# Performance work log

Measured on AMD Instinct MI355X. Metric: run time of the kernel, lower is better.

The kernel has to match this reference:

```python
import jax, jax.numpy as jnp
import numpy as np

B, N = 4, 1024
DIM, DEPTH, HEADS, DHEAD, MLP = 512, 6, 8, 64, 2048
INNER = HEADS * DHEAD
SCALE = DHEAD ** -0.5
EPS = 1e-5


def setup_inputs() -> dict:
    key = jax.random.key(0)
    ks = jax.random.split(key, 16)
    w = lambda k, shape: (jax.random.normal(k, shape, jnp.float32) * 0.02)
    D = DEPTH
    return {
        "g": jax.random.normal(ks[0], (B, N, DIM), jnp.float32),
        "x": jax.random.normal(ks[1], (B, N, DIM), jnp.float32),
        # PreNorm + SelfAttention
        "ln1_s": jnp.ones((D, DIM)), "ln1_b": jnp.zeros((D, DIM)),
        "Wqkv": w(ks[2], (D, DIM, 3 * INNER)),
        "Wo_sa": w(ks[3], (D, INNER, DIM)), "bo_sa": jnp.zeros((D, DIM)),
        # RelationalCrossAttention
        "lng_s": jnp.ones((D, DIM)), "lng_b": jnp.zeros((D, DIM)),
        "lnx_s": jnp.ones((D, DIM)), "lnx_b": jnp.zeros((D, DIM)),
        "Wq": w(ks[4], (D, DIM, INNER)),
        "Wk": w(ks[5], (D, DIM, INNER)),
        "Wv": w(ks[6], (D, DIM, INNER)), "bv": jnp.zeros((D, INNER)),
        "Wo_ca": w(ks[7], (D, INNER, DIM)), "bo_ca": jnp.zeros((D, DIM)),
        # PreNorm + FeedForward (same module applied twice per layer)
        "lnf_s": jnp.ones((D, DIM)), "lnf_b": jnp.zeros((D, DIM)),
        "W1": w(ks[8], (D, DIM, MLP)), "b1": jnp.zeros((D, MLP)),
        "W2": w(ks[9], (D, MLP, DIM)), "b2": jnp.zeros((D, DIM)),
    }


def _ln(t, s, b):
    m = t.mean(-1, keepdims=True)
    v = ((t - m) ** 2).mean(-1, keepdims=True)
    return (t - m) / jnp.sqrt(v + EPS) * s + b


def _split_heads(t):  # [b, n, h*d] -> [b, h, n, d]
    b, n, _ = t.shape
    return t.reshape(b, n, HEADS, DHEAD).transpose(0, 2, 1, 3)


def _merge_heads(t):  # [b, h, n, d] -> [b, n, h*d]
    b, h, n, d = t.shape
    return t.transpose(0, 2, 1, 3).reshape(b, n, h * d)


def _attend(q, k, v):
    dots = jnp.einsum('bhnd,bhmd->bhnm', q, k) * SCALE
    attn = jax.nn.softmax(jnp.nan_to_num(dots, nan=-jnp.inf), axis=-1)
    attn = jnp.nan_to_num(attn)  # nan_to_num(0.0) post-softmax as in source
    return jnp.einsum('bhnm,bhmd->bhnd', attn, jnp.nan_to_num(v))


def reference(g, x, ln1_s, ln1_b, Wqkv, Wo_sa, bo_sa, lng_s, lng_b, lnx_s, lnx_b,
              Wq, Wk, Wv, bv, Wo_ca, bo_ca, lnf_s, lnf_b, W1, b1, W2, b2):
    for i in range(DEPTH):
        def ff(t):
            h = jax.nn.gelu(_ln(t, lnf_s[i], lnf_b[i]) @ W1[i] + b1[i], approximate=False)
            return h @ W2[i] + b2[i]
        # relational cross attention: q,k from g, v from x
        gn = _ln(g, lng_s[i], lng_b[i])
        xn = _ln(x, lnx_s[i], lnx_b[i])
        q = _split_heads(gn @ Wq[i])
        k = _split_heads(gn @ Wk[i])
        v = _split_heads(xn @ Wv[i] + bv[i])
        x = _merge_heads(_attend(q, k, v)) @ Wo_ca[i] + bo_ca[i] + x
        x = ff(x) + x
        # pre-norm self attention (skip connection enabled)
        sn = _ln(x, ln1_s[i], ln1_b[i])
        qkv = sn @ Wqkv[i]
        qs, ks_, vs = jnp.split(qkv, 3, axis=-1)
        sa = _merge_heads(_attend(_split_heads(qs), _split_heads(ks_), _split_heads(vs)))
        x = sa @ Wo_sa[i] + bo_sa[i] + x
        x = ff(x) + x
    return x
```

## Files before the change

kernel.cpp:

```cpp
#include <hip/hip_runtime.h>
#include <hip/hip_bf16.h>
#include <cstdint>
#include <cstddef>

#define DEV __device__ __forceinline__

using f32x4 = __attribute__((ext_vector_type(4))) float;
using bfx8  = __attribute__((ext_vector_type(8))) __bf16;
using s16x8 = __attribute__((ext_vector_type(8))) short;

DEV uint16_t f2bf(float f) {
    union { float f; uint32_t u; } x; x.f = f;
    uint32_t r = x.u + 0x7fffu + ((x.u >> 16) & 1u);
    return (uint16_t)(r >> 16);
}

DEV float gelu_exact(float v) {
    return 0.5f * v * (1.0f + erff(v * 0.70710678118654752f));
}

DEV f32x4 mfma16(s16x8 a, s16x8 b, f32x4 c) {
    return __builtin_amdgcn_mfma_f32_16x16x32_bf16(
        __builtin_bit_cast(bfx8, a), __builtin_bit_cast(bfx8, b), c, 0, 0, 0);
}

DEV void async_lds16(const void* g, void* l) {
    __builtin_amdgcn_global_load_lds(
        (const __attribute__((address_space(1))) uint32_t*)g,
        (__attribute__((address_space(3))) uint32_t*)l, 16, 0, 0);
}

template<int N> DEV void wait_vmcnt() {
    if constexpr (N == 0)      asm volatile("s_waitcnt vmcnt(0)" ::: "memory");
    else if constexpr (N == 4) asm volatile("s_waitcnt vmcnt(4)" ::: "memory");
    else static_assert(N == 0 || N == 4, "add vmcnt literal");
}
#define SBAR      asm volatile("s_barrier" ::: "memory")
#define LGKM0     asm volatile("s_waitcnt lgkmcnt(0)" ::: "memory")
#define SCHED0    __builtin_amdgcn_sched_barrier(0)

DEV void ln_row(const float* __restrict__ in, const float* __restrict__ sc,
                const float* __restrict__ bi, uint16_t* __restrict__ out, size_t row)
{
    const int lane = threadIdx.x & 63;
    const float* p = in + row * 512 + lane * 8;
    float4 a = *(const float4*)p;
    float4 b4 = *(const float4*)(p + 4);
    float v[8] = {a.x, a.y, a.z, a.w, b4.x, b4.y, b4.z, b4.w};
    float s = 0.f, sq = 0.f;
#pragma unroll
    for (int j = 0; j < 8; ++j) { s += v[j]; sq += v[j] * v[j]; }
#pragma unroll
    for (int o = 1; o < 64; o <<= 1) { s += __shfl_xor(s, o); sq += __shfl_xor(sq, o); }
    const float mean = s * (1.0f / 512.0f);
    const float var  = sq * (1.0f / 512.0f) - mean * mean;
    const float rstd = rsqrtf(var + 1e-5f);
    const int c = lane * 8;
    uint16_t o8[8];
#pragma unroll
    for (int j = 0; j < 8; ++j)
        o8[j] = f2bf((v[j] - mean) * rstd * sc[c + j] + bi[c + j]);
    uint4 pk;
    pk.x = (uint32_t)o8[0] | ((uint32_t)o8[1] << 16);
    pk.y = (uint32_t)o8[2] | ((uint32_t)o8[3] << 16);
    pk.z = (uint32_t)o8[4] | ((uint32_t)o8[5] << 16);
    pk.w = (uint32_t)o8[6] | ((uint32_t)o8[7] << 16);
    *reinterpret_cast<uint4*>(out + row * 512 + c) = pk;
}

__global__ __launch_bounds__(256)
void ln_bf16(const float* __restrict__ in, const float* __restrict__ sc,
             const float* __restrict__ bi, uint16_t* __restrict__ out)
{
    ln_row(in, sc, bi, out, (size_t)blockIdx.x * 4 + (threadIdx.x >> 6));
}

__global__ __launch_bounds__(256)
void ln2_bf16(const float* __restrict__ in0, const float* __restrict__ sc0,
              const float* __restrict__ bi0, uint16_t* __restrict__ out0,
              const float* __restrict__ in1, const float* __restrict__ sc1,
              const float* __restrict__ bi1, uint16_t* __restrict__ out1)
{
    const int sel = blockIdx.x >> 10;
    const size_t row = (size_t)(blockIdx.x & 1023) * 4 + (threadIdx.x >> 6);
    if (sel == 0) ln_row(in0, sc0, bi0, out0, row);
    else          ln_row(in1, sc1, bi1, out1, row);
}

__global__ __launch_bounds__(256)
void wtrans(const float* __restrict__ W, uint16_t* __restrict__ WT, int K, int N,
            size_t lstride, int row0)
{
    __shared__ float tile[32][33];
    const int l = blockIdx.z;
    const int k0 = blockIdx.x * 32, n0 = blockIdx.y * 32;
    const float* Wl = W + (size_t)l * K * N;
    uint16_t* WTl = WT + (size_t)l * lstride;
    const int tx = threadIdx.x, ty = threadIdx.y;
#pragma unroll
    for (int j = 0; j < 4; ++j)
        tile[ty + j * 8][tx] = Wl[(size_t)(k0 + ty + j * 8) * N + n0 + tx];
    __syncthreads();
#pragma unroll
    for (int j = 0; j < 4; ++j)
        WTl[(size_t)(row0 + n0 + ty + j * 8) * K + k0 + tx] = f2bf(tile[tx][ty + j * 8]);
}

__global__ __launch_bounds__(256)
void vtrans(const uint16_t* __restrict__ src, uint16_t* __restrict__ vt, int C, int coff)
{
    __shared__ uint16_t tile[64][72];
    const int n0 = blockIdx.x * 64;
    const int bh = blockIdx.y, b = bh >> 3, h = bh & 7;
    const int tx = threadIdx.x, ty = threadIdx.y;
#pragma unroll
    for (int j = 0; j < 16; ++j) {
        const int n = ty + j * 4;
        tile[n][tx] = src[((size_t)b * 1024 + n0 + n) * C + coff + h * 64 + tx];
    }
    __syncthreads();
    uint16_t* o = vt + (size_t)bh * 65536;
#pragma unroll
    for (int j = 0; j < 16; ++j) {
        const int d = ty + j * 4;
        o[(size_t)d * 1024 + n0 + tx] = tile[tx][d];
    }
}

template<int BM, int BN, int NWR, int NWC, int MINW,
         int HAS_BIAS, int HAS_RESID, int DO_GELU, int OUT_BF16, int PARTIAL>
__global__ __launch_bounds__(NWR * NWC * 64, MINW)
void gemm5(const uint16_t* __restrict__ A, const uint16_t* __restrict__ BT,
           const float* __restrict__ bias, const float* __restrict__ resid,
           void* __restrict__ outp, int M, int N, int K, int kh)
{
    constexpr int NT = NWR * NWC * 64;
    constexpr int WM = BM / NWR, WN = BN / NWC;
    constexpr int FM = WM / 16, FN = WN / 16;
    constexpr int ASLOTS = 8 * BM, BSLOTS = 8 * BN, TOT = ASLOTS + BSLOTS;
    constexpr int S = TOT / NT;
    static_assert(S == 4, "vmcnt literal assumes S==4");
    __shared__ uint16_t As[2][ASLOTS * 8];
    __shared__ uint16_t Bs[2][BSLOTS * 8];
    const int tid = threadIdx.x, lane = tid & 63;
    const int w = tid >> 6, wr = w / NWC, wc = w % NWC;
    const int kg = lane >> 4, lr = lane & 15;
    const int nwg = gridDim.x;
    const int id0 = blockIdx.x;
    const int id = (id0 & 7) * (nwg >> 3) + (id0 >> 3);
    const int nbn = N / BN;
    const size_t m0 = (size_t)(id / nbn) * BM;
    const size_t n0 = (size_t)(id % nbn) * BN;
    const int kbase = PARTIAL ? blockIdx.y * kh : 0;

    auto stage = [&](int b, int k0) {
#pragma unroll
        for (int j = 0; j < S; ++j) {
            const int s = j * NT + tid;
            if (s < ASLOTS) {
                const int sub = s / BM, row = s % BM;
                async_lds16(A + (m0 + row) * K + k0 + sub * 8, &As[b][s * 8]);
            } else {
                const int s2 = s - ASLOTS;
                const int sub = s2 / BN, row = s2 % BN;
                async_lds16(BT + (n0 + row) * K + k0 + sub * 8, &Bs[b][s2 * 8]);
            }
        }
    };

    f32x4 acc[FM][FN] = {};
    const int nt = kh / 64;
    stage(0, kbase);
    stage(1, kbase + 64);
    int cur = 0;
    for (int t = 0; t < nt; ++t) {
        if (t < nt - 1) wait_vmcnt<S>(); else wait_vmcnt<0>();
        SBAR;
        s16x8 af[2][FM], bf[2][FN];
#pragma unroll
        for (int ks = 0; ks < 2; ++ks) {
#pragma unroll
            for (int i = 0; i < FM; ++i)
                af[ks][i] = *(const s16x8*)&As[cur][((ks * 4 + kg) * BM + wr * WM + i * 16 + lr) * 8];
#pragma unroll
            for (int j = 0; j < FN; ++j)
                bf[ks][j] = *(const s16x8*)&Bs[cur][((ks * 4 + kg) * BN + wc * WN + j * 16 + lr) * 8];
        }
        __builtin_amdgcn_s_setprio(1);
#pragma unroll
        for (int ks = 0; ks < 2; ++ks)
#pragma unroll
            for (int i = 0; i < FM; ++i)
#pragma unroll
                for (int j = 0; j < FN; ++j)
                    acc[i][j] = mfma16(af[ks][i], bf[ks][j], acc[i][j]);
        __builtin_amdgcn_s_setprio(0);
        LGKM0; SCHED0;
        SBAR;
        if (t + 2 < nt) stage(cur, kbase + (t + 2) * 64);
        cur ^= 1;
    }
    float* pout = PARTIAL ? (float*)outp + (size_t)blockIdx.y * M * (size_t)N : nullptr;
#pragma unroll
    for (int i = 0; i < FM; ++i) {
        const size_t rbase = m0 + wr * WM + i * 16 + kg * 4;
#pragma unroll
        for (int j = 0; j < FN; ++j) {
            const size_t col = n0 + wc * WN + j * 16 + lr;
            const float bval = HAS_BIAS ? bias[col] : 0.0f;
#pragma unroll
            for (int r = 0; r < 4; ++r) {
                const size_t row = rbase + r;
                float v = acc[i][j][r] + bval;
                if (PARTIAL) { pout[row * (size_t)N + col] = v; continue; }
                if (DO_GELU)  v = gelu_exact(v);
                if (HAS_RESID) v += resid[row * (size_t)N + col];
                if (OUT_BF16) ((uint16_t*)outp)[row * (size_t)N + col] = f2bf(v);
                else          ((float*)outp)[row * (size_t)N + col] = v;
            }
        }
    }
}

__global__ __launch_bounds__(256)
void reduce2(const float* __restrict__ p, const float* __restrict__ bias,
             float* __restrict__ x)
{
    const size_t i = ((size_t)blockIdx.x * 256 + threadIdx.x) * 8;
    const int col = (int)(i & 511);
    const float* q = p + 4096ull * 512;
    float4 a0 = *(const float4*)(p + i),     a1 = *(const float4*)(p + i + 4);
    float4 b0 = *(const float4*)(q + i),     b1 = *(const float4*)(q + i + 4);
    float4 s0 = *(const float4*)(bias + col), s1 = *(const float4*)(bias + col + 4);
    float4 r0 = *(const float4*)(x + i),     r1 = *(const float4*)(x + i + 4);
    float4 o0, o1;
    o0.x = a0.x + b0.x + s0.x + r0.x;  o0.y = a0.y + b0.y + s0.y + r0.y;
    o0.z = a0.z + b0.z + s0.z + r0.z;  o0.w = a0.w + b0.w + s0.w + r0.w;
    o1.x = a1.x + b1.x + s1.x + r1.x;  o1.y = a1.y + b1.y + s1.y + r1.y;
    o1.z = a1.z + b1.z + s1.z + r1.z;  o1.w = a1.w + b1.w + s1.w + r1.w;
    *(float4*)(x + i) = o0;
    *(float4*)(x + i + 4) = o1;
}

__global__ __launch_bounds__(256)
void attn_flash(const uint16_t* __restrict__ Qb, const uint16_t* __restrict__ Kb,
                const uint16_t* __restrict__ Vt, uint16_t* __restrict__ Ob,
                int qstride, int kstride, int qoff, int koff)
{
    __shared__ uint16_t Ks[2][4096];
    __shared__ uint16_t Vs[2][4096];
    __shared__ uint16_t Pb[4][1024];
    const int tid = threadIdx.x, lane = tid & 63, w = tid >> 6;
    const int kg = lane >> 4, lr = lane & 15;
    const int bh = blockIdx.y, b = bh >> 3, h = bh & 7;
    const int q0 = blockIdx.x * 64;
    const float CEXP = 0.125f * 1.44269504f;

    s16x8 aq0, aq1;
    {
        const size_t qrow = (size_t)b * 1024 + q0 + w * 16 + lr;
        const uint16_t* qp = Qb + qrow * qstride + qoff + h * 64 + kg * 8;
        aq0 = *(const s16x8*)qp;
        aq1 = *(const s16x8*)(qp + 32);
    }
    const uint16_t* kbase = Kb + (size_t)b * 1024 * kstride + koff + h * 64;
    const uint16_t* vbase = Vt + (size_t)bh * 65536;

    float l_r[4] = {0.f, 0.f, 0.f, 0.f};
    f32x4 acc[4] = {};

    auto stage = [&](int buf, int kv0) {
#pragma unroll
        for (int j = 0; j < 2; ++j) {
            const int s = j * 256 + tid;
            const int sub = s >> 6, row = s & 63;
            async_lds16(kbase + (size_t)(kv0 + row) * kstride + sub * 8, &Ks[buf][s * 8]);
            async_lds16(vbase + (size_t)row * 1024 + kv0 + sub * 8,      &Vs[buf][s * 8]);
        }
    };

    stage(0, 0);
    __syncthreads();
    int cur = 0;
    for (int t = 0; t < 16; ++t) {
        if (t < 15) stage(cur ^ 1, (t + 1) * 64);
        f32x4 s4[4];
        __builtin_amdgcn_s_setprio(1);
#pragma unroll
        for (int ni = 0; ni < 4; ++ni) {
            s16x8 bk0 = *(const s16x8*)&Ks[cur][(kg * 64 + ni * 16 + lr) * 8];
            s16x8 bk1 = *(const s16x8*)&Ks[cur][((4 + kg) * 64 + ni * 16 + lr) * 8];
            f32x4 z = {};
            z = mfma16(aq0, bk0, z);
            z = mfma16(aq1, bk1, z);
            s4[ni] = z;
        }
        __builtin_amdgcn_s_setprio(0);
#pragma unroll
        for (int ni = 0; ni < 4; ++ni) {
            const int slotb = (ni * 2 + (lr >> 3)) * 16 + kg * 4;
#pragma unroll
            for (int r = 0; r < 4; ++r) {
                const float pe = __builtin_amdgcn_exp2f(s4[ni][r] * CEXP);
                l_r[r] += pe;
                Pb[w][(slotb + r) * 8 + (lr & 7)] = f2bf(pe);
            }
        }
        s16x8 ap0 = *(const s16x8*)&Pb[w][(kg * 16 + lr) * 8];
        s16x8 ap1 = *(const s16x8*)&Pb[w][((4 + kg) * 16 + lr) * 8];
        __builtin_amdgcn_s_setprio(1);
#pragma unroll
        for (int ni = 0; ni < 4; ++ni) {
            s16x8 bv0 = *(const s16x8*)&Vs[cur][(kg * 64 + ni * 16 + lr) * 8];
            s16x8 bv1 = *(const s16x8*)&Vs[cur][((4 + kg) * 64 + ni * 16 + lr) * 8];
            acc[ni] = mfma16(ap0, bv0, acc[ni]);
            acc[ni] = mfma16(ap1, bv1, acc[ni]);
        }
        __builtin_amdgcn_s_setprio(0);
        __syncthreads();
        cur ^= 1;
    }
    float linv[4];
#pragma unroll
    for (int r = 0; r < 4; ++r) {
        float l = l_r[r];
        l += __shfl_xor(l, 1); l += __shfl_xor(l, 2);
        l += __shfl_xor(l, 4); l += __shfl_xor(l, 8);
        linv[r] = 1.0f / l;
    }
#pragma unroll
    for (int ni = 0; ni < 4; ++ni)
#pragma unroll
        for (int r = 0; r < 4; ++r) {
            const float v = acc[ni][r] * linv[r];
            const size_t row = (size_t)b * 1024 + q0 + w * 16 + kg * 4 + r;
            Ob[row * 512 + h * 64 + ni * 16 + lr] = f2bf(v);
        }
}

extern "C" void kernel_launch(void* const* d_in, const int* in_sizes, int n_in,
                              void* d_out, int out_size, void* d_ws, size_t ws_size,
                              hipStream_t stream)
{
    (void)in_sizes; (void)n_in; (void)out_size; (void)ws_size;
    const float* g     = (const float*)d_in[0];
    const float* x0    = (const float*)d_in[1];
    const float* ln1_s = (const float*)d_in[2];
    const float* ln1_b = (const float*)d_in[3];
    const float* Wqkv  = (const float*)d_in[4];
    const float* Wo_sa = (const float*)d_in[5];
    const float* bo_sa = (const float*)d_in[6];
    const float* lng_s = (const float*)d_in[7];
    const float* lng_b = (const float*)d_in[8];
    const float* lnx_s = (const float*)d_in[9];
    const float* lnx_b = (const float*)d_in[10];
    const float* Wq    = (const float*)d_in[11];
    const float* Wk    = (const float*)d_in[12];
    const float* Wv    = (const float*)d_in[13];
    const float* bv    = (const float*)d_in[14];
    const float* Wo_ca = (const float*)d_in[15];
    const float* bo_ca = (const float*)d_in[16];
    const float* lnf_s = (const float*)d_in[17];
    const float* lnf_b = (const float*)d_in[18];
    const float* W1    = (const float*)d_in[19];
    const float* b1    = (const float*)d_in[20];
    const float* W2    = (const float*)d_in[21];
    const float* b2    = (const float*)d_in[22];

    float* x = (float*)d_out;

    char* p = (char*)d_ws;
    auto carve = [&](size_t n) { char* r = p; p += (n + 255) & ~(size_t)255; return r; };
    uint16_t* WqkT  = (uint16_t*)carve(6ull * 1024 * 512 * 2);
    uint16_t* WvT   = (uint16_t*)carve(6ull * 512 * 512 * 2);
    uint16_t* WocaT = (uint16_t*)carve(6ull * 512 * 512 * 2);
    uint16_t* WqkvT = (uint16_t*)carve(6ull * 1536 * 512 * 2);
    uint16_t* WosaT = (uint16_t*)carve(6ull * 512 * 512 * 2);
    uint16_t* W1T   = (uint16_t*)carve(6ull * 2048 * 512 * 2);
    uint16_t* W2T   = (uint16_t*)carve(6ull * 512 * 2048 * 2);
    uint16_t* gn    = (uint16_t*)carve(4096ull * 512 * 2);
    uint16_t* xn    = (uint16_t*)carve(4096ull * 512 * 2);
    uint16_t* qkvu  = (uint16_t*)carve(4096ull * 1536 * 2);
    uint16_t* vt    = (uint16_t*)carve(32ull * 64 * 1024 * 2);
    uint16_t* ab    = (uint16_t*)carve(4096ull * 512 * 2);
    uint16_t* hb    = (uint16_t*)carve(4096ull * 2048 * 2);
    float*    pk2   = (float*)carve(2ull * 4096 * 512 * 4);
    uint16_t* qk = qkvu;
    uint16_t* vb = qkvu + 4096ull * 1024;

    dim3 tb(32, 8);
    wtrans<<<dim3(16, 16, 6), tb, 0, stream>>>(Wq,    WqkT,  512, 512,  1024ull * 512, 0);
    wtrans<<<dim3(16, 16, 6), tb, 0, stream>>>(Wk,    WqkT,  512, 512,  1024ull * 512, 512);
    wtrans<<<dim3(16, 16, 6), tb, 0, stream>>>(Wv,    WvT,   512, 512,  512ull * 512, 0);
    wtrans<<<dim3(16, 16, 6), tb, 0, stream>>>(Wo_ca, WocaT, 512, 512,  512ull * 512, 0);
    wtrans<<<dim3(16, 48, 6), tb, 0, stream>>>(Wqkv,  WqkvT, 512, 1536, 1536ull * 512, 0);
    wtrans<<<dim3(16, 16, 6), tb, 0, stream>>>(Wo_sa, WosaT, 512, 512,  512ull * 512, 0);
    wtrans<<<dim3(16, 64, 6), tb, 0, stream>>>(W1,    W1T,   512, 2048, 2048ull * 512, 0);
    wtrans<<<dim3(64, 16, 6), tb, 0, stream>>>(W2,    W2T,   2048, 512, 2048ull * 512, 0);

    hipMemcpyAsync(x, x0, 4096ull * 512 * 4, hipMemcpyDeviceToDevice, stream);

    const dim3 ga(16, 32), va(16, 32), vb4(64, 4);

    for (int l = 0; l < 6; ++l) {
        const size_t o512 = (size_t)l * 512, oW = (size_t)l * 512 * 512;
        const size_t oW1 = (size_t)l * 2048 * 512, oWqkv = (size_t)l * 1536 * 512;
        const size_t o2048 = (size_t)l * 2048;

        ln2_bf16<<<2048, 256, 0, stream>>>(g, lng_s + o512, lng_b + o512, gn,
                                           x, lnx_s + o512, lnx_b + o512, xn);
        gemm5<128, 128, 2, 4, 4, 0, 0, 0, 1, 0><<<256, 512, 0, stream>>>(
            gn, WqkT + (size_t)l * 1024 * 512, nullptr, nullptr, qk, 4096, 1024, 512, 512);
        gemm5<64, 64, 2, 2, 4, 1, 0, 0, 1, 0><<<512, 256, 0, stream>>>(
            xn, WvT + oW, bv + o512, nullptr, vb, 4096, 512, 512, 512);
        vtrans<<<va, vb4, 0, stream>>>(vb, vt, 512, 0);
        attn_flash<<<ga, 256, 0, stream>>>(qk, qk, vt, ab, 1024, 1024, 0, 512);
        gemm5<64, 64, 2, 2, 4, 1, 1, 0, 0, 0><<<512, 256, 0, stream>>>(
            ab, WocaT + oW, bo_ca + o512, x, x, 4096, 512, 512, 512);

        ln_bf16<<<1024, 256, 0, stream>>>(x, lnf_s + o512, lnf_b + o512, xn);
        gemm5<64, 64, 2, 2, 4, 1, 0, 1, 1, 0><<<2048, 256, 0, stream>>>(
            xn, W1T + oW1, b1 + o2048, nullptr, hb, 4096, 2048, 512, 512);
        gemm5<64, 64, 2, 2, 4, 0, 0, 0, 0, 1><<<dim3(512, 2), 256, 0, stream>>>(
            hb, W2T + oW1, nullptr, nullptr, pk2, 4096, 512, 2048, 1024);
        reduce2<<<1024, 256, 0, stream>>>(pk2, b2 + o512, x);

        ln_bf16<<<1024, 256, 0, stream>>>(x, ln1_s + o512, ln1_b + o512, xn);
        gemm5<128, 128, 2, 4, 4, 0, 0, 0, 1, 0><<<384, 512, 0, stream>>>(
            xn, WqkvT + oWqkv, nullptr, nullptr, qkvu, 4096, 1536, 512, 512);
        vtrans<<<va, vb4, 0, stream>>>(qkvu, vt, 1536, 1024);
        attn_flash<<<ga, 256, 0, stream>>>(qkvu, qkvu, vt, ab, 1536, 1536, 0, 512);
        gemm5<64, 64, 2, 2, 4, 1, 1, 0, 0, 0><<<512, 256, 0, stream>>>(
            ab, WosaT + oW, bo_sa + o512, x, x, 4096, 512, 512, 512);

        ln_bf16<<<1024, 256, 0, stream>>>(x, lnf_s + o512, lnf_b + o512, xn);
        gemm5<64, 64, 2, 2, 4, 1, 0, 1, 1, 0><<<2048, 256, 0, stream>>>(
            xn, W1T + oW1, b1 + o2048, nullptr, hb, 4096, 2048, 512, 512);
        gemm5<64, 64, 2, 2, 4, 0, 0, 0, 0, 1><<<dim3(512, 2), 256, 0, stream>>>(
            hb, W2T + oW1, nullptr, nullptr, pk2, 4096, 512, 2048, 1024);
        reduce2<<<1024, 256, 0, stream>>>(pk2, b2 + o512, x);
    }
}
```

Before: 1.826 ms.

## Hoist g-side QK projections for all layers, fuse V transpose and reduce+LN

The layer norm of g is computed once without scale and bias. Those per-layer affine terms are folded into the Wq/Wk weights and a precomputed bias, so a single large GEMM produces the Q and K for all six layers up front. The V-projection GEMMs now write the transposed V layout directly from their epilogues, which removes the vtrans kernels. The FF residual reduction is fused with the next layer norm, and the W1 GEMM moves to 128x128 tiles. Together these cut kernel launches and intermediate round trips, at the cost of a large extra qkall buffer and slightly different bf16 rounding from the weight folding.

```diff
diff --git a/kernel.cpp b/kernel.cpp
--- a/kernel.cpp
+++ b/kernel.cpp
@@ -39,10 +39,13 @@
 #define LGKM0     asm volatile("s_waitcnt lgkmcnt(0)" ::: "memory")
 #define SCHED0    __builtin_amdgcn_sched_barrier(0)
 
-DEV void ln_row(const float* __restrict__ in, const float* __restrict__ sc,
-                const float* __restrict__ bi, uint16_t* __restrict__ out, size_t row)
+template<int HAS_SB>
+__global__ __launch_bounds__(256)
+void ln_t(const float* __restrict__ in, const float* __restrict__ sc,
+          const float* __restrict__ bi, uint16_t* __restrict__ out)
 {
     const int lane = threadIdx.x & 63;
+    const size_t row = (size_t)blockIdx.x * 4 + (threadIdx.x >> 6);
     const float* p = in + row * 512 + lane * 8;
     float4 a = *(const float4*)p;
     float4 b4 = *(const float4*)(p + 4);
@@ -58,8 +61,11 @@
     const int c = lane * 8;
     uint16_t o8[8];
 #pragma unroll
-    for (int j = 0; j < 8; ++j)
-        o8[j] = f2bf((v[j] - mean) * rstd * sc[c + j] + bi[c + j]);
+    for (int j = 0; j < 8; ++j) {
+        float z = (v[j] - mean) * rstd;
+        if (HAS_SB) z = z * sc[c + j] + bi[c + j];
+        o8[j] = f2bf(z);
+    }
     uint4 pk;
     pk.x = (uint32_t)o8[0] | ((uint32_t)o8[1] << 16);
     pk.y = (uint32_t)o8[2] | ((uint32_t)o8[3] << 16);
@@ -69,27 +75,8 @@
 }
 
 __global__ __launch_bounds__(256)
-void ln_bf16(const float* __restrict__ in, const float* __restrict__ sc,
-             const float* __restrict__ bi, uint16_t* __restrict__ out)
-{
-    ln_row(in, sc, bi, out, (size_t)blockIdx.x * 4 + (threadIdx.x >> 6));
-}
-
-__global__ __launch_bounds__(256)
-void ln2_bf16(const float* __restrict__ in0, const float* __restrict__ sc0,
-              const float* __restrict__ bi0, uint16_t* __restrict__ out0,
-              const float* __restrict__ in1, const float* __restrict__ sc1,
-              const float* __restrict__ bi1, uint16_t* __restrict__ out1)
-{
-    const int sel = blockIdx.x >> 10;
-    const size_t row = (size_t)(blockIdx.x & 1023) * 4 + (threadIdx.x >> 6);
-    if (sel == 0) ln_row(in0, sc0, bi0, out0, row);
-    else          ln_row(in1, sc1, bi1, out1, row);
-}
-
-__global__ __launch_bounds__(256)
 void wtrans(const float* __restrict__ W, uint16_t* __restrict__ WT, int K, int N,
-            size_t lstride, int row0)
+            size_t lstride, int row0, const float* __restrict__ kscale)
 {
     __shared__ float tile[32][33];
     const int l = blockIdx.z;
@@ -98,8 +85,12 @@
     uint16_t* WTl = WT + (size_t)l * lstride;
     const int tx = threadIdx.x, ty = threadIdx.y;
 #pragma unroll
-    for (int j = 0; j < 4; ++j)
-        tile[ty + j * 8][tx] = Wl[(size_t)(k0 + ty + j * 8) * N + n0 + tx];
+    for (int j = 0; j < 4; ++j) {
+        const int k = k0 + ty + j * 8;
+        float w = Wl[(size_t)k * N + n0 + tx];
+        if (kscale) w *= kscale[l * K + k];
+        tile[ty + j * 8][tx] = w;
+    }
     __syncthreads();
 #pragma unroll
     for (int j = 0; j < 4; ++j)
@@ -107,32 +98,25 @@
 }
 
 __global__ __launch_bounds__(256)
-void vtrans(const uint16_t* __restrict__ src, uint16_t* __restrict__ vt, int C, int coff)
-{
-    __shared__ uint16_t tile[64][72];
-    const int n0 = blockIdx.x * 64;
-    const int bh = blockIdx.y, b = bh >> 3, h = bh & 7;
-    const int tx = threadIdx.x, ty = threadIdx.y;
-#pragma unroll
-    for (int j = 0; j < 16; ++j) {
-        const int n = ty + j * 4;
-        tile[n][tx] = src[((size_t)b * 1024 + n0 + n) * C + coff + h * 64 + tx];
-    }
-    __syncthreads();
-    uint16_t* o = vt + (size_t)bh * 65536;
-#pragma unroll
-    for (int j = 0; j < 16; ++j) {
-        const int d = ty + j * 4;
-        o[(size_t)d * 1024 + n0 + tx] = tile[tx][d];
-    }
+void bfold(const float* __restrict__ b, const float* __restrict__ Wq,
+           const float* __restrict__ Wk, float* __restrict__ out)
+{
+    const int n = blockIdx.x * 256 + threadIdx.x;
+    const int l = blockIdx.y, sel = blockIdx.z;
+    const float* bb = b + l * 512;
+    const float* W = (sel ? Wk : Wq) + (size_t)l * 512 * 512;
+    float s = 0.f;
+    for (int k = 0; k < 512; ++k) s += bb[k] * W[(size_t)k * 512 + n];
+    out[l * 1024 + sel * 512 + n] = s;
 }
 
 template<int BM, int BN, int NWR, int NWC, int MINW,
-         int HAS_BIAS, int HAS_RESID, int DO_GELU, int OUT_BF16, int PARTIAL>
+         int HAS_BIAS, int HAS_RESID, int DO_GELU, int OUT_BF16, int PARTIAL, int OUT_VT>
 __global__ __launch_bounds__(NWR * NWC * 64, MINW)
-void gemm5(const uint16_t* __restrict__ A, const uint16_t* __restrict__ BT,
+void gemm6(const uint16_t* __restrict__ A, const uint16_t* __restrict__ BT,
            const float* __restrict__ bias, const float* __restrict__ resid,
-           void* __restrict__ outp, int M, int N, int K, int kh)
+           void* __restrict__ outp, uint16_t* __restrict__ vt,
+           int M, int N, int K, int kh)
 {
     constexpr int NT = NWR * NWC * 64;
     constexpr int WM = BM / NWR, WN = BN / NWC;
@@ -200,6 +184,27 @@
         if (t + 2 < nt) stage(cur, kbase + (t + 2) * 64);
         cur ^= 1;
     }
+    if (OUT_VT == 1 || (OUT_VT == 2 && n0 >= 1024)) {
+#pragma unroll
+        for (int i = 0; i < FM; ++i) {
+            const size_t rbase = m0 + wr * WM + i * 16 + kg * 4;
+            const int b = (int)(rbase >> 10), nloc = (int)(rbase & 1023);
+#pragma unroll
+            for (int j = 0; j < FN; ++j) {
+                const int col = (int)n0 + wc * WN + j * 16 + lr;
+                const int c2 = (OUT_VT == 2) ? col - 1024 : col;
+                const float bval = HAS_BIAS ? bias[c2] : 0.0f;
+                const int h = c2 >> 6, d = c2 & 63;
+                ushort4 pk;
+                pk.x = f2bf(acc[i][j][0] + bval);
+                pk.y = f2bf(acc[i][j][1] + bval);
+                pk.z = f2bf(acc[i][j][2] + bval);
+                pk.w = f2bf(acc[i][j][3] + bval);
+                *(ushort4*)&vt[((size_t)(b * 8 + h) * 64 + d) * 1024 + nloc] = pk;
+            }
+        }
+        return;
+    }
     float* pout = PARTIAL ? (float*)outp + (size_t)blockIdx.y * M * (size_t)N : nullptr;
 #pragma unroll
     for (int i = 0; i < FM; ++i) {
@@ -222,24 +227,49 @@
     }
 }
 
+template<int DO_LN>
 __global__ __launch_bounds__(256)
-void reduce2(const float* __restrict__ p, const float* __restrict__ bias,
-             float* __restrict__ x)
-{
-    const size_t i = ((size_t)blockIdx.x * 256 + threadIdx.x) * 8;
-    const int col = (int)(i & 511);
-    const float* q = p + 4096ull * 512;
-    float4 a0 = *(const float4*)(p + i),     a1 = *(const float4*)(p + i + 4);
-    float4 b0 = *(const float4*)(q + i),     b1 = *(const float4*)(q + i + 4);
-    float4 s0 = *(const float4*)(bias + col), s1 = *(const float4*)(bias + col + 4);
-    float4 r0 = *(const float4*)(x + i),     r1 = *(const float4*)(x + i + 4);
-    float4 o0, o1;
-    o0.x = a0.x + b0.x + s0.x + r0.x;  o0.y = a0.y + b0.y + s0.y + r0.y;
-    o0.z = a0.z + b0.z + s0.z + r0.z;  o0.w = a0.w + b0.w + s0.w + r0.w;
-    o1.x = a1.x + b1.x + s1.x + r1.x;  o1.y = a1.y + b1.y + s1.y + r1.y;
-    o1.z = a1.z + b1.z + s1.z + r1.z;  o1.w = a1.w + b1.w + s1.w + r1.w;
-    *(float4*)(x + i) = o0;
-    *(float4*)(x + i + 4) = o1;
+void reduce_ln(const float* __restrict__ p, const float* __restrict__ bias,
+               float* __restrict__ x, const float* __restrict__ sc,
+               const float* __restrict__ bi, uint16_t* __restrict__ xn)
+{
+    const int lane = threadIdx.x & 63;
+    const size_t row = (size_t)blockIdx.x * 4 + (threadIdx.x >> 6);
+    const int c = lane * 8;
+    const size_t off = row * 512 + c;
+    const float* p0 = p + off;
+    const float* p1 = p + 4096ull * 512 + off;
+    float4 a0 = *(const float4*)p0,        a1 = *(const float4*)(p0 + 4);
+    float4 b0 = *(const float4*)p1,        b1 = *(const float4*)(p1 + 4);
+    float4 s0 = *(const float4*)(bias + c), s1 = *(const float4*)(bias + c + 4);
+    float4 r0 = *(const float4*)(x + off), r1 = *(const float4*)(x + off + 4);
+    float v[8];
+    v[0] = a0.x + b0.x + s0.x + r0.x;  v[1] = a0.y + b0.y + s0.y + r0.y;
+    v[2] = a0.z + b0.z + s0.z + r0.z;  v[3] = a0.w + b0.w + s0.w + r0.w;
+    v[4] = a1.x + b1.x + s1.x + r1.x;  v[5] = a1.y + b1.y + s1.y + r1.y;
+    v[6] = a1.z + b1.z + s1.z + r1.z;  v[7] = a1.w + b1.w + s1.w + r1.w;
+    *(float4*)(x + off)     = make_float4(v[0], v[1], v[2], v[3]);
+    *(float4*)(x + off + 4) = make_float4(v[4], v[5], v[6], v[7]);
+    if (DO_LN) {
+        float s = 0.f, sq = 0.f;
+#pragma unroll
+        for (int j = 0; j < 8; ++j) { s += v[j]; sq += v[j] * v[j]; }
+#pragma unroll
+        for (int o = 1; o < 64; o <<= 1) { s += __shfl_xor(s, o); sq += __shfl_xor(sq, o); }
+        const float mean = s * (1.0f / 512.0f);
+        const float var  = sq * (1.0f / 512.0f) - mean * mean;
+        const float rstd = rsqrtf(var + 1e-5f);
+        uint16_t o8[8];
+#pragma unroll
+        for (int j = 0; j < 8; ++j)
+            o8[j] = f2bf((v[j] - mean) * rstd * sc[c + j] + bi[c + j]);
+        uint4 pk;
+        pk.x = (uint32_t)o8[0] | ((uint32_t)o8[1] << 16);
+        pk.y = (uint32_t)o8[2] | ((uint32_t)o8[3] << 16);
+        pk.z = (uint32_t)o8[4] | ((uint32_t)o8[5] << 16);
+        pk.w = (uint32_t)o8[6] | ((uint32_t)o8[7] << 16);
+        *reinterpret_cast<uint4*>(xn + off) = pk;
+    }
 }
 
 __global__ __launch_bounds__(256)
@@ -378,66 +408,72 @@
     uint16_t* WosaT = (uint16_t*)carve(6ull * 512 * 512 * 2);
     uint16_t* W1T   = (uint16_t*)carve(6ull * 2048 * 512 * 2);
     uint16_t* W2T   = (uint16_t*)carve(6ull * 512 * 2048 * 2);
-    uint16_t* gn    = (uint16_t*)carve(4096ull * 512 * 2);
+    float*    bqk   = (float*)carve(6144ull * 4);
+    uint16_t* zg    = (uint16_t*)carve(4096ull * 512 * 2);
+    uint16_t* qkall = (uint16_t*)carve(4096ull * 6144 * 2);
     uint16_t* xn    = (uint16_t*)carve(4096ull * 512 * 2);
     uint16_t* qkvu  = (uint16_t*)carve(4096ull * 1536 * 2);
     uint16_t* vt    = (uint16_t*)carve(32ull * 64 * 1024 * 2);
     uint16_t* ab    = (uint16_t*)carve(4096ull * 512 * 2);
     uint16_t* hb    = (uint16_t*)carve(4096ull * 2048 * 2);
     float*    pk2   = (float*)carve(2ull * 4096 * 512 * 4);
-    uint16_t* qk = qkvu;
-    uint16_t* vb = qkvu + 4096ull * 1024;
 
     dim3 tb(32, 8);
-    wtrans<<<dim3(16, 16, 6), tb, 0, stream>>>(Wq,    WqkT,  512, 512,  1024ull * 512, 0);
-    wtrans<<<dim3(16, 16, 6), tb, 0, stream>>>(Wk,    WqkT,  512, 512,  1024ull * 512, 512);
-    wtrans<<<dim3(16, 16, 6), tb, 0, stream>>>(Wv,    WvT,   512, 512,  512ull * 512, 0);
-    wtrans<<<dim3(16, 16, 6), tb, 0, stream>>>(Wo_ca, WocaT, 512, 512,  512ull * 512, 0);
-    wtrans<<<dim3(16, 48, 6), tb, 0, stream>>>(Wqkv,  WqkvT, 512, 1536, 1536ull * 512, 0);
-    wtrans<<<dim3(16, 16, 6), tb, 0, stream>>>(Wo_sa, WosaT, 512, 512,  512ull * 512, 0);
-    wtrans<<<dim3(16, 64, 6), tb, 0, stream>>>(W1,    W1T,   512, 2048, 2048ull * 512, 0);
-    wtrans<<<dim3(64, 16, 6), tb, 0, stream>>>(W2,    W2T,   2048, 512, 2048ull * 512, 0);
+    wtrans<<<dim3(16, 16, 6), tb, 0, stream>>>(Wq,    WqkT,  512, 512,  1024ull * 512, 0,   lng_s);
+    wtrans<<<dim3(16, 16, 6), tb, 0, stream>>>(Wk,    WqkT,  512, 512,  1024ull * 512, 512, lng_s);
+    wtrans<<<dim3(16, 16, 6), tb, 0, stream>>>(Wv,    WvT,   512, 512,  512ull * 512, 0, nullptr);
+    wtrans<<<dim3(16, 16, 6), tb, 0, stream>>>(Wo_ca, WocaT, 512, 512,  512ull * 512, 0, nullptr);
+    wtrans<<<dim3(16, 48, 6), tb, 0, stream>>>(Wqkv,  WqkvT, 512, 1536, 1536ull * 512, 0, nullptr);
+    wtrans<<<dim3(16, 16, 6), tb, 0, stream>>>(Wo_sa, WosaT, 512, 512,  512ull * 512, 0, nullptr);
+    wtrans<<<dim3(16, 64, 6), tb, 0, stream>>>(W1,    W1T,   512, 2048, 2048ull * 512, 0, nullptr);
+    wtrans<<<dim3(64, 16, 6), tb, 0, stream>>>(W2,    W2T,   2048, 512, 2048ull * 512, 0, nullptr);
+    bfold<<<dim3(2, 6, 2), 256, 0, stream>>>(lng_b, Wq, Wk, bqk);
 
     hipMemcpyAsync(x, x0, 4096ull * 512 * 4, hipMemcpyDeviceToDevice, stream);
 
-    const dim3 ga(16, 32), va(16, 32), vb4(64, 4);
+    ln_t<0><<<1024, 256, 0, stream>>>(g, nullptr, nullptr, zg);
+    ln_t<1><<<1024, 256, 0, stream>>>(x, lnx_s, lnx_b, xn);
+    gemm6<128, 128, 2, 4, 4, 1, 0, 0, 1, 0, 0><<<1536, 512, 0, stream>>>(
+        zg, WqkT, bqk, nullptr, qkall, nullptr, 4096, 6144, 512, 512);
+
+    const dim3 ga(16, 32);
 
     for (int l = 0; l < 6; ++l) {
         const size_t o512 = (size_t)l * 512, oW = (size_t)l * 512 * 512;
         const size_t oW1 = (size_t)l * 2048 * 512, oWqkv = (size_t)l * 1536 * 512;
         const size_t o2048 = (size_t)l * 2048;
 
-        ln2_bf16<<<2048, 256, 0, stream>>>(g, lng_s + o512, lng_b + o512, gn,
-                                           x, lnx_s + o512, lnx_b + o512, xn);
-        gemm5<128, 128, 2, 4, 4, 0, 0, 0, 1, 0><<<256, 512, 0, stream>>>(
-            gn, WqkT + (size_t)l * 1024 * 512, nullptr, nullptr, qk, 4096, 1024, 512, 512);
-        gemm5<64, 64, 2, 2, 4, 1, 0, 0, 1, 0><<<512, 256, 0, stream>>>(
-            xn, WvT + oW, bv + o512, nullptr, vb, 4096, 512, 512, 512);
-        vtrans<<<va, vb4, 0, stream>>>(vb, vt, 512, 0);
-        attn_flash<<<ga, 256, 0, stream>>>(qk, qk, vt, ab, 1024, 1024, 0, 512);
-        gemm5<64, 64, 2, 2, 4, 1, 1, 0, 0, 0><<<512, 256, 0, stream>>>(
-            ab, WocaT + oW, bo_ca + o512, x, x, 4096, 512, 512, 512);
-
-        ln_bf16<<<1024, 256, 0, stream>>>(x, lnf_s + o512, lnf_b + o512, xn);
-        gemm5<64, 64, 2, 2, 4, 1, 0, 1, 1, 0><<<2048, 256, 0, stream>>>(
-            xn, W1T + oW1, b1 + o2048, nullptr, hb, 4096, 2048, 512, 512);
-        gemm5<64, 64, 2, 2, 4, 0, 0, 0, 0, 1><<<dim3(512, 2), 256, 0, stream>>>(
-            hb, W2T + oW1, nullptr, nullptr, pk2, 4096, 512, 2048, 1024);
-        reduce2<<<1024, 256, 0, stream>>>(pk2, b2 + o512, x);
-
-        ln_bf16<<<1024, 256, 0, stream>>>(x, ln1_s + o512, ln1_b + o512, xn);
-        gemm5<128, 128, 2, 4, 4, 0, 0, 0, 1, 0><<<384, 512, 0, stream>>>(
-            xn, WqkvT + oWqkv, nullptr, nullptr, qkvu, 4096, 1536, 512, 512);
-        vtrans<<<va, vb4, 0, stream>>>(qkvu, vt, 1536, 1024);
+        gemm6<64, 64, 2, 2, 4, 1, 0, 0, 0, 0, 1><<<512, 256, 0, stream>>>(
+            xn, WvT + oW, bv + o512, nullptr, nullptr, vt, 4096, 512, 512, 512);
+        attn_flash<<<ga, 256, 0, stream>>>(qkall, qkall, vt, ab, 6144, 6144,
+                                           l * 1024, l * 1024 + 512);
+        gemm6<64, 64, 2, 2, 4, 1, 1, 0, 0, 0, 0><<<512, 256, 0, stream>>>(
+            ab, WocaT + oW, bo_ca + o512, x, x, nullptr, 4096, 512, 512, 512);
+
+        ln_t<1><<<1024, 256, 0, stream>>>(x, lnf_s + o512, lnf_b + o512, xn);
+        gemm6<128, 128, 2, 4, 4, 1, 0, 1, 1, 0, 0><<<512, 512, 0, stream>>>(
+            xn, W1T + oW1, b1 + o2048, nullptr, hb, nullptr, 4096, 2048, 512, 512);
+        gemm6<64, 64, 2, 2, 4, 0, 0, 0, 0, 1, 0><<<dim3(512, 2), 256, 0, stream>>>(
+            hb, W2T + oW1, nullptr, nullptr, pk2, nullptr, 4096, 512, 2048, 1024);
+        reduce_ln<1><<<1024, 256, 0, stream>>>(pk2, b2 + o512, x,
+                                               ln1_s + o512, ln1_b + o512, xn);
+
+        gemm6<128, 128, 2, 4, 4, 0, 0, 0, 1, 0, 2><<<384, 512, 0, stream>>>(
+            xn, WqkvT + oWqkv, nullptr, nullptr, qkvu, vt, 4096, 1536, 512, 512);
         attn_flash<<<ga, 256, 0, stream>>>(qkvu, qkvu, vt, ab, 1536, 1536, 0, 512);
-        gemm5<64, 64, 2, 2, 4, 1, 1, 0, 0, 0><<<512, 256, 0, stream>>>(
-            ab, WosaT + oW, bo_sa + o512, x, x, 4096, 512, 512, 512);
-
-        ln_bf16<<<1024, 256, 0, stream>>>(x, lnf_s + o512, lnf_b + o512, xn);
-        gemm5<64, 64, 2, 2, 4, 1, 0, 1, 1, 0><<<2048, 256, 0, stream>>>(
-            xn, W1T + oW1, b1 + o2048, nullptr, hb, 4096, 2048, 512, 512);
-        gemm5<64, 64, 2, 2, 4, 0, 0, 0, 0, 1><<<dim3(512, 2), 256, 0, stream>>>(
-            hb, W2T + oW1, nullptr, nullptr, pk2, 4096, 512, 2048, 1024);
-        reduce2<<<1024, 256, 0, stream>>>(pk2, b2 + o512, x);
-    }
-}
+        gemm6<64, 64, 2, 2, 4, 1, 1, 0, 0, 0, 0><<<512, 256, 0, stream>>>(
+            ab, WosaT + oW, bo_sa + o512, x, x, nullptr, 4096, 512, 512, 512);
+
+        ln_t<1><<<1024, 256, 0, stream>>>(x, lnf_s + o512, lnf_b + o512, xn);
+        gemm6<128, 128, 2, 4, 4, 1, 0, 1, 1, 0, 0><<<512, 512, 0, stream>>>(
+            xn, W1T + oW1, b1 + o2048, nullptr, hb, nullptr, 4096, 2048, 512, 512);
+        gemm6<64, 64, 2, 2, 4, 0, 0, 0, 0, 1, 0><<<dim3(512, 2), 256, 0, stream>>>(
+            hb, W2T + oW1, nullptr, nullptr, pk2, nullptr, 4096, 512, 2048, 1024);
+        if (l < 5)
+            reduce_ln<1><<<1024, 256, 0, stream>>>(pk2, b2 + o512, x,
+                                                   lnx_s + o512 + 512, lnx_b + o512 + 512, xn);
+        else
+            reduce_ln<0><<<1024, 256, 0, stream>>>(pk2, b2 + o512, x,
+                                                   nullptr, nullptr, nullptr);
+    }
+}
```

Result: faster. 1.649 ms (-9.7%).
